# Kernel optimization log

Hardware: AMD Instinct MI355X
Metric: run time of the kernel (lower is better)

Reference implementation:

```python
import jax, jax.numpy as jnp
import numpy as np

KSTRIDE = (16, 16)  # matches init_kwargs kstride


def setup_inputs() -> dict:
    key = jax.random.key(0)
    k1, k2, k3, k4, k5 = jax.random.split(key, 5)
    B, C, H, W = 4, 64, 512, 512
    N, kh, kw = 2048, 16, 16
    sh, sw = KSTRIDE
    inp = jax.random.normal(k1, (B, C, H, W), dtype=jnp.float32)
    gathered = jax.random.normal(k2, (N, C, kh, kw), dtype=jnp.float32)
    # valid block coords: h0*sh + kh <= H  ->  h0 in [0, H//sh) since kh == sh
    bi = jax.random.randint(k3, (N,), 0, B)
    hi = jax.random.randint(k4, (N,), 0, H // sh)
    wi = jax.random.randint(k5, (N,), 0, W // sw)
    indices = jnp.stack([bi, hi, wi], axis=1).astype(jnp.int64)
    return {"input": inp, "gathered": gathered, "indices": indices}


def reference(input, gathered, indices):
    # Vectorized scatter-add of N patches [C, kh, kw] into input [B, C, H, W]
    # at strided block offsets. Duplicated indices accumulate (+=), matching
    # the original in-place loop.
    sh, sw = KSTRIDE
    N, C, kh, kw = gathered.shape
    b = indices[:, 0][:, None, None]                                   # [N,1,1]
    r = (indices[:, 1] * sh)[:, None, None] + jnp.arange(kh)[None, :, None]  # [N,kh,1]
    c = (indices[:, 2] * sw)[:, None, None] + jnp.arange(kw)[None, None, :]  # [N,1,kw]
    x = jnp.transpose(input, (0, 2, 3, 1))      # [B,H,W,C] so C is a trailing slice
    g = jnp.transpose(gathered, (0, 2, 3, 1))   # [N,kh,kw,C]
    x = x.at[b, r, c, :].add(g)                 # scatter-add over all N blocks at once
    return jnp.transpose(x, (0, 3, 1, 2))       # back to [B,C,H,W]
```

## Files before the change

### kernel.cpp

```cpp
#include <hip/hip_runtime.h>

#define BB 4
#define CC 64
#define HH 512
#define WW 512
#define NN 2048
#define SLOTS 4096


__global__ __launch_bounds__(1024) void prelude_kernel(const int* __restrict__ idx,
                                                       int* __restrict__ heads,
                                                       int* __restrict__ nxt) {
    __shared__ int s_is64;
    const int t = threadIdx.x;
    if (t == 0) s_is64 = 1;

    #pragma unroll
    for (int i = t; i < SLOTS; i += 1024) heads[i] = -1;
    __syncthreads();

    for (int i = t; i < 3 * NN / 2; i += 1024) {
        if (idx[2 * i + 1] != 0) s_is64 = 0;
    }
    __syncthreads();

    const bool is64 = (s_is64 != 0);
    for (int n = t; n < NN; n += 1024) {
        int b, hi, wi;
        if (is64) {
            b  = idx[6 * n + 0];
            hi = idx[6 * n + 2];
            wi = idx[6 * n + 4];
        } else {
            b  = idx[3 * n + 0];
            hi = idx[3 * n + 1];
            wi = idx[3 * n + 2];
        }
        const int slot = (b << 10) | (hi << 5) | wi;
        nxt[n] = atomicExch(&heads[slot], n);
    }
}

__global__ __launch_bounds__(256) void scatter_add_kernel(
    const float4* __restrict__ in4,
    const float4* __restrict__ g4,
    const int* __restrict__ heads,
    const int* __restrict__ nxt,
    float4* __restrict__ out4)
{
    const int t  = blockIdx.x * 256 + threadIdx.x;
    const int w4 = t & 127;
    const int hq = (t >> 7) & 127;
    const int cb = t >> 14;
    const int c  = cb & 63;
    const int b  = cb >> 6;
    const int h0 = hq << 2;

    const int base = (cb << 16) | (h0 << 7) | w4;

    float4 v0 = in4[base];
    float4 v1 = in4[base + 128];
    float4 v2 = in4[base + 256];
    float4 v3 = in4[base + 384];

    const int slot = (b << 10) | ((hq >> 2) << 5) | (w4 >> 2);
    int n = heads[slot];
    if (n >= 0) {
        const int goff = (c << 6) | ((h0 & 15) << 2) | (w4 & 3);
        do {
            const float4* __restrict__ gp = g4 + ((n << 12) + goff);
            const float4 g0 = gp[0];
            const float4 g1 = gp[4];
            const float4 g2 = gp[8];
            const float4 g3 = gp[12];
            const int nn = nxt[n];
            v0.x += g0.x; v0.y += g0.y; v0.z += g0.z; v0.w += g0.w;
            v1.x += g1.x; v1.y += g1.y; v1.z += g1.z; v1.w += g1.w;
            v2.x += g2.x; v2.y += g2.y; v2.z += g2.z; v2.w += g2.w;
            v3.x += g3.x; v3.y += g3.y; v3.z += g3.z; v3.w += g3.w;
            n = nn;
        } while (n >= 0);
    }

    out4[base]       = v0;
    out4[base + 128] = v1;
    out4[base + 256] = v2;
    out4[base + 384] = v3;
}

__global__ __launch_bounds__(256) void copy_kernel(const float4* __restrict__ in4,
                                                   float4* __restrict__ out4) {
    int e = blockIdx.x * 256 + threadIdx.x;
    out4[e] = in4[e];
}

__global__ __launch_bounds__(256) void atomic_scatter_kernel(
    const float* __restrict__ g,
    const int* __restrict__ idx,
    float* __restrict__ out)
{
    int i = blockIdx.x * 256 + threadIdx.x;
    int n = i >> 14;
    int r = i & 16383;
    int c  = r >> 8;
    int rr = (r >> 4) & 15;
    int w  = r & 15;
    int b  = idx[3 * n + 0];
    int hi = idx[3 * n + 1];
    int wi = idx[3 * n + 2];
    int off = ((b * CC + c) * HH + hi * 16 + rr) * WW + wi * 16 + w;
    atomicAdd(&out[off], g[i]);
}

extern "C" void kernel_launch(void* const* d_in, const int* in_sizes, int n_in,
                              void* d_out, int out_size, void* d_ws, size_t ws_size,
                              hipStream_t stream) {
    const float* inp      = (const float*)d_in[0];
    const float* gathered = (const float*)d_in[1];
    const int*   idx      = (const int*)d_in[2];
    float* out = (float*)d_out;

    const size_t ws_needed = (size_t)(SLOTS + NN) * sizeof(int);

    if (ws_size >= ws_needed) {
        int* heads = (int*)d_ws;
        int* nxt   = heads + SLOTS;
        prelude_kernel<<<1, 1024, 0, stream>>>(idx, heads, nxt);
        const int n_thr = BB * CC * (HH / 4) * (WW / 4);
        scatter_add_kernel<<<n_thr / 256, 256, 0, stream>>>(
            (const float4*)inp, (const float4*)gathered, heads, nxt, (float4*)out);
    } else {
        const int n_out4 = BB * CC * HH * (WW / 4);
        copy_kernel<<<n_out4 / 256, 256, 0, stream>>>((const float4*)inp, (float4*)out);
        const int n_g = NN * CC * 16 * 16;
        atomic_scatter_kernel<<<n_g / 256, 256, 0, stream>>>(gathered, idx, out);
    }
}
```

Baseline: 517.7 us.

## Replace per-slot linked lists with fixed-capacity index arrays and nontemporal accesses

The prelude now builds per-slot bounded arrays of patch indices in shared memory, with a linked-list overflow beyond 16 entries. The scatter kernel reads those arrays and loads two patches per iteration, replacing the serial dependent chase through the next pointers. Input, gathered and output traffic now uses nontemporal loads and stores to reduce cache pollution on the streaming data. The cost is a larger workspace and extra shared-memory work in the single-block prelude.

Result: faster. 500.8 us (-3.3%).

```diff
diff --git a/kernel.cpp b/kernel.cpp
--- a/kernel.cpp
+++ b/kernel.cpp
@@ -6,17 +6,23 @@
 #define WW 512
 #define NN 2048
 #define SLOTS 4096
+#define CAP 16
+
+typedef float vf4 __attribute__((ext_vector_type(4)));
 
 
 __global__ __launch_bounds__(1024) void prelude_kernel(const int* __restrict__ idx,
+                                                       int* __restrict__ lst,
+                                                       int* __restrict__ cnts,
                                                        int* __restrict__ heads,
                                                        int* __restrict__ nxt) {
+    __shared__ int s_cnt[SLOTS];
+    __shared__ int s_head[SLOTS];
     __shared__ int s_is64;
     const int t = threadIdx.x;
     if (t == 0) s_is64 = 1;
 
-    #pragma unroll
-    for (int i = t; i < SLOTS; i += 1024) heads[i] = -1;
+    for (int i = t; i < SLOTS; i += 1024) { s_cnt[i] = 0; s_head[i] = -1; }
     __syncthreads();
 
     for (int i = t; i < 3 * NN / 2; i += 1024) {
@@ -37,16 +43,23 @@
             wi = idx[3 * n + 2];
         }
         const int slot = (b << 10) | (hi << 5) | wi;
-        nxt[n] = atomicExch(&heads[slot], n);
+        const int pos  = atomicAdd(&s_cnt[slot], 1);
+        if (pos < CAP) lst[(slot << 4) + pos] = n;
+        else           nxt[n] = atomicExch(&s_head[slot], n);
     }
+    __syncthreads();
+
+    for (int i = t; i < SLOTS; i += 1024) { cnts[i] = s_cnt[i]; heads[i] = s_head[i]; }
 }
 
 __global__ __launch_bounds__(256) void scatter_add_kernel(
-    const float4* __restrict__ in4,
-    const float4* __restrict__ g4,
+    const vf4* __restrict__ in4,
+    const vf4* __restrict__ g4,
+    const int* __restrict__ lst,
+    const int* __restrict__ cnts,
     const int* __restrict__ heads,
     const int* __restrict__ nxt,
-    float4* __restrict__ out4)
+    vf4* __restrict__ out4)
 {
     const int t  = blockIdx.x * 256 + threadIdx.x;
     const int w4 = t & 127;
@@ -56,40 +69,72 @@
     const int b  = cb >> 6;
     const int h0 = hq << 2;
 
+    const int slot = (b << 10) | ((hq >> 2) << 5) | (w4 >> 2);
+    const int cnt  = cnts[slot];
+
     const int base = (cb << 16) | (h0 << 7) | w4;
 
-    float4 v0 = in4[base];
-    float4 v1 = in4[base + 128];
-    float4 v2 = in4[base + 256];
-    float4 v3 = in4[base + 384];
+    vf4 v0 = __builtin_nontemporal_load(&in4[base]);
+    vf4 v1 = __builtin_nontemporal_load(&in4[base + 128]);
+    vf4 v2 = __builtin_nontemporal_load(&in4[base + 256]);
+    vf4 v3 = __builtin_nontemporal_load(&in4[base + 384]);
 
-    const int slot = (b << 10) | ((hq >> 2) << 5) | (w4 >> 2);
-    int n = heads[slot];
-    if (n >= 0) {
-        const int goff = (c << 6) | ((h0 & 15) << 2) | (w4 & 3);
-        do {
-            const float4* __restrict__ gp = g4 + ((n << 12) + goff);
-            const float4 g0 = gp[0];
-            const float4 g1 = gp[4];
-            const float4 g2 = gp[8];
-            const float4 g3 = gp[12];
-            const int nn = nxt[n];
-            v0.x += g0.x; v0.y += g0.y; v0.z += g0.z; v0.w += g0.w;
-            v1.x += g1.x; v1.y += g1.y; v1.z += g1.z; v1.w += g1.w;
-            v2.x += g2.x; v2.y += g2.y; v2.z += g2.z; v2.w += g2.w;
-            v3.x += g3.x; v3.y += g3.y; v3.z += g3.z; v3.w += g3.w;
-            n = nn;
-        } while (n >= 0);
+    if (cnt > 0) {
+        const int goff  = (c << 6) | ((h0 & 15) << 2) | (w4 & 3);
+        const int lbase = slot << 4;
+        const int cnt16 = cnt < CAP ? cnt : CAP;
+        int i = 0;
+        for (; i + 2 <= cnt16; i += 2) {
+            const int n0 = lst[lbase + i];
+            const int n1 = lst[lbase + i + 1];
+            const vf4* __restrict__ gp0 = g4 + ((n0 << 12) + goff);
+            const vf4* __restrict__ gp1 = g4 + ((n1 << 12) + goff);
+            const vf4 a0 = __builtin_nontemporal_load(gp0 + 0);
+            const vf4 a1 = __builtin_nontemporal_load(gp0 + 4);
+            const vf4 a2 = __builtin_nontemporal_load(gp0 + 8);
+            const vf4 a3 = __builtin_nontemporal_load(gp0 + 12);
+            const vf4 b0 = __builtin_nontemporal_load(gp1 + 0);
+            const vf4 b1 = __builtin_nontemporal_load(gp1 + 4);
+            const vf4 b2 = __builtin_nontemporal_load(gp1 + 8);
+            const vf4 b3 = __builtin_nontemporal_load(gp1 + 12);
+            v0 += a0 + b0;
+            v1 += a1 + b1;
+            v2 += a2 + b2;
+            v3 += a3 + b3;
+        }
+        if (i < cnt16) {
+            const int n0 = lst[lbase + i];
+            const vf4* __restrict__ gp0 = g4 + ((n0 << 12) + goff);
+            v0 += __builtin_nontemporal_load(gp0 + 0);
+            v1 += __builtin_nontemporal_load(gp0 + 4);
+            v2 += __builtin_nontemporal_load(gp0 + 8);
+            v3 += __builtin_nontemporal_load(gp0 + 12);
+        }
+        if (cnt > CAP) {
+            int n = heads[slot];
+            while (n >= 0) {
+                const vf4* __restrict__ gp = g4 + ((n << 12) + goff);
+                const vf4 a0 = gp[0];
+                const vf4 a1 = gp[4];
+                const vf4 a2 = gp[8];
+                const vf4 a3 = gp[12];
+                n = nxt[n];
+                v0 += a0;
+                v1 += a1;
+                v2 += a2;
+                v3 += a3;
+            }
+        }
     }
 
-    out4[base]       = v0;
-    out4[base + 128] = v1;
-    out4[base + 256] = v2;
-    out4[base + 384] = v3;
+    __builtin_nontemporal_store(v0, &out4[base]);
+    __builtin_nontemporal_store(v1, &out4[base + 128]);
+    __builtin_nontemporal_store(v2, &out4[base + 256]);
+    __builtin_nontemporal_store(v3, &out4[base + 384]);
 }
 
-__global__ __launch_bounds__(256) void copy_kernel(const float4* __restrict__ in4,
-                                                   float4* __restrict__ out4) {
+__global__ __launch_bounds__(256) void copy_kernel(const vf4* __restrict__ in4,
+                                                   vf4* __restrict__ out4) {
     int e = blockIdx.x * 256 + threadIdx.x;
     out4[e] = in4[e];
 }
@@ -120,18 +165,21 @@
     const int*   idx      = (const int*)d_in[2];
     float* out = (float*)d_out;
 
-    const size_t ws_needed = (size_t)(SLOTS + NN) * sizeof(int);
+    const size_t ws_needed = (size_t)(SLOTS * CAP + SLOTS + SLOTS + NN) * sizeof(int);
 
     if (ws_size >= ws_needed) {
-        int* heads = (int*)d_ws;
+        int* lst   = (int*)d_ws;
+        int* cnts  = lst + SLOTS * CAP;
+        int* heads = cnts + SLOTS;
         int* nxt   = heads + SLOTS;
-        prelude_kernel<<<1, 1024, 0, stream>>>(idx, heads, nxt);
+        prelude_kernel<<<1, 1024, 0, stream>>>(idx, lst, cnts, heads, nxt);
         const int n_thr = BB * CC * (HH / 4) * (WW / 4);
         scatter_add_kernel<<<n_thr / 256, 256, 0, stream>>>(
-            (const float4*)inp, (const float4*)gathered, heads, nxt, (float4*)out);
+            (const vf4*)inp, (const vf4*)gathered, lst, cnts, heads, nxt,
+            (vf4*)out);
     } else {
         const int n_out4 = BB * CC * HH * (WW / 4);
-        copy_kernel<<<n_out4 / 256, 256, 0, stream>>>((const float4*)inp, (float4*)out);
+        copy_kernel<<<n_out4 / 256, 256, 0, stream>>>((const vf4*)inp, (vf4*)out);
         const int n_g = NN * CC * 16 * 16;
         atomic_scatter_kernel<<<n_g / 256, 256, 0, stream>>>(gathered, idx, out);
     }
```
